# Kernel tuning notes

Measured on AMD Instinct MI355X. Metric: run time of the kernel, lower is better.

The kernel has to match this reference:

```python
import jax, jax.numpy as jnp
import numpy as np
import math

B, S, D, H, DH, DFF = 2, 2048, 2048, 16, 128, 8192
EPS = 1e-6
K_AMB = -1.0


def log_map_origin(x, K):
    # x: (..., d+1) Lorentz point -> tangent vector (..., d)
    xi = x[..., 1:]
    n = jnp.sqrt(jnp.sum(xi * xi, axis=-1, keepdims=True))
    a = jnp.sqrt(-K) * n
    # asinh(a)/a, stable near 0 (on-manifold, acosh(sqrt(-K)x0) == asinh(sqrt(-K)||xi||))
    f = jnp.where(a < 1e-6, 1.0 - a * a / 6.0, jnp.arcsinh(a) / jnp.maximum(a, 1e-12))
    return f * xi


def exp_map_stable(v, K):
    # v: (..., d) tangent -> Lorentz point (..., d+1); x0 from exact constraint
    n = jnp.sqrt(jnp.sum(v * v, axis=-1, keepdims=True))
    a = jnp.sqrt(-K) * n
    sinc = jnp.where(a < 1e-6, 1.0 + a * a / 6.0, jnp.sinh(a) / jnp.maximum(a, 1e-12))
    xi = sinc * v
    x0 = jnp.sqrt(-1.0 / K + jnp.sum(xi * xi, axis=-1, keepdims=True))
    return jnp.concatenate([x0, xi], axis=-1)


def lorentz_rmsnorm(x, scale):
    v = log_map_origin(x, K_AMB)
    rms = jnp.sqrt(jnp.mean(v * v, axis=-1, keepdims=True) + EPS)
    return exp_map_stable(scale * (v / rms), K_AMB)


def per_head_attention(x_normed, mask, Wq, Wk, Wv, Wo, head_K):
    v = log_map_origin(x_normed, K_AMB)  # (B,S,D)
    def split(w):
        return (v @ w).reshape(B, S, H, DH).transpose(0, 2, 1, 3)  # (B,H,S,DH)
    q, k, vv = split(Wq), split(Wk), split(Wv)
    Kh = head_K[None, :, None, None]  # (1,H,1,1) per-head curvature
    ql = exp_map_stable(q, Kh)  # (B,H,S,DH+1)
    kl = exp_map_stable(k, Kh)
    # Lorentz inner product <q,k>_L = -q0 k0 + qi.ki via signed metric
    metric = jnp.concatenate([-jnp.ones((1,)), jnp.ones((DH,))])
    L = jnp.einsum('bhqd,bhkd->bhqk', ql * metric, kl)
    # negative squared-distance proxy: 2<q,k>_L - 2/K  (zero when q==k)
    scores = (2.0 * L - 2.0 / Kh) / math.sqrt(DH)
    scores = jnp.where(mask[None, None, :, :], scores, -1e30)
    attn = jax.nn.softmax(scores, axis=-1)
    out = jnp.einsum('bhqk,bhkd->bhqd', attn, vv)  # (B,H,S,DH)
    out = out.transpose(0, 2, 1, 3).reshape(B, S, H * DH)
    return out @ Wo  # Euclidean (B,S,D)


def block_forward(x, mask, scale1, scale2, Wq, Wk, Wv, Wo, head_K, W1, W2):
    xn = lorentz_rmsnorm(x, scale1)
    attn_out = per_head_attention(xn, mask, Wq, Wk, Wv, Wo, head_K)
    x = exp_map_stable(log_map_origin(x, K_AMB) + attn_out, K_AMB)
    xn = lorentz_rmsnorm(x, scale2)
    vf = log_map_origin(xn, K_AMB)
    ffn_eu_pre = jax.nn.gelu(vf @ W1, approximate=False) @ W2
    ffn_out = exp_map_stable(ffn_eu_pre, K_AMB)
    x = exp_map_stable(log_map_origin(x, K_AMB) + log_map_origin(ffn_out, K_AMB), K_AMB)
    return x


def setup_inputs() -> dict:
    key = jax.random.key(0)
    ks = jax.random.split(key, 9)
    v0 = jax.random.normal(ks[0], (B, S, D), jnp.float32) * 0.02
    x = exp_map_stable(v0, K_AMB)  # on-manifold input (B,S,D+1)
    mask = jnp.tril(jnp.ones((S, S), bool))  # causal: True = attend
    init_scale = 1.0 / math.sqrt(D)
    w_std = 0.02
    return {
        'x': x,
        'mask': mask,
        'scale1': jnp.full((D,), init_scale, jnp.float32),
        'scale2': jnp.full((D,), init_scale, jnp.float32),
        'Wq': jax.random.normal(ks[1], (D, H * DH), jnp.float32) * w_std,
        'Wk': jax.random.normal(ks[2], (D, H * DH), jnp.float32) * w_std,
        'Wv': jax.random.normal(ks[3], (D, H * DH), jnp.float32) * w_std,
        'Wo': jax.random.normal(ks[4], (H * DH, D), jnp.float32) * w_std,
        'head_K': jnp.full((H,), -1.0, jnp.float32),
        'W1': jax.random.normal(ks[5], (D, DFF), jnp.float32) * w_std,
        'W2': jax.random.normal(ks[6], (DFF, D), jnp.float32) * w_std,
    }


def reference(x, mask, scale1, scale2, Wq, Wk, Wv, Wo, head_K, W1, W2):
    return block_forward(x, mask, scale1, scale2, Wq, Wk, Wv, Wo, head_K, W1, W2)
```

## Files before the change

### kernel.cpp

```cpp
#include <hip/hip_runtime.h>
#include <stdint.h>

typedef unsigned short u16;
typedef __attribute__((ext_vector_type(8))) short bf16x8;
typedef __attribute__((ext_vector_type(4))) float f32x4;

#define SEQ    2048
#define NB     2
#define NHEAD  16
#define DHEAD  128
#define DMODEL 2048
#define DFFN   8192
#define MROWS  4096

__device__ __forceinline__ u16 f2bf(float x) {
  union { float f; uint32_t u; } v; v.f = x;
  return (u16)((v.u + 0x7fffu + ((v.u >> 16) & 1u)) >> 16);
}
__device__ __forceinline__ float bf2f(u16 h) {
  union { uint32_t u; float f; } v; v.u = ((uint32_t)h) << 16;
  return v.f;
}
__device__ __forceinline__ void gload16(const void* g, void* l) {
  __builtin_amdgcn_global_load_lds((const __attribute__((address_space(1))) void*)g,
                                   (__attribute__((address_space(3))) void*)l,
                                   16, 0, 0);
}
__device__ __forceinline__ float blockSum256(float v) {
  __shared__ float red[4];
  #pragma unroll
  for (int m = 1; m < 64; m <<= 1) v += __shfl_xor(v, m, 64);
  int w = threadIdx.x >> 6;
  if ((threadIdx.x & 63) == 0) red[w] = v;
  __syncthreads();
  float s = red[0] + red[1] + red[2] + red[3];
  __syncthreads();
  return s;
}

__global__ void transpose_w(const float* __restrict__ in, u16* __restrict__ out, int R, int C) {
  __shared__ float tile[32][33];
  int c0 = blockIdx.x * 32, r0 = blockIdx.y * 32;
  int tx = threadIdx.x, ty = threadIdx.y;
  #pragma unroll
  for (int i = 0; i < 4; ++i)
    tile[ty + 8*i][tx] = in[(size_t)(r0 + ty + 8*i) * C + c0 + tx];
  __syncthreads();
  #pragma unroll
  for (int i = 0; i < 4; ++i)
    out[(size_t)(c0 + ty + 8*i) * R + r0 + tx] = f2bf(tile[tx][ty + 8*i]);
}

__global__ void ln_first(const float* __restrict__ x, const float* __restrict__ scale,
                         float* __restrict__ v1, u16* __restrict__ t1) {
  int row = blockIdx.x;
  const float* xr = x + (size_t)row * (DMODEL + 1) + 1;
  float vals[8]; float ss = 0.f;
  #pragma unroll
  for (int i = 0; i < 8; ++i) {
    int idx = threadIdx.x + 256 * i;
    vals[i] = xr[idx];
    ss += vals[i] * vals[i];
  }
  ss = blockSum256(ss);
  float n = sqrtf(ss);
  float f = (n < 1e-6f) ? (1.0f - n * n * (1.0f/6.0f)) : (asinhf(n) / n);
  float rms = sqrtf(f * f * ss * (1.0f / DMODEL) + 1e-6f);
  float ir = 1.0f / rms;
  #pragma unroll
  for (int i = 0; i < 8; ++i) {
    int idx = threadIdx.x + 256 * i;
    float v = f * vals[i];
    v1[(size_t)row * DMODEL + idx] = v;
    t1[(size_t)row * DMODEL + idx] = f2bf(scale[idx] * v * ir);
  }
}

__global__ void rms_mid(const float* __restrict__ u, const float* __restrict__ scale,
                        u16* __restrict__ t) {
  int row = blockIdx.x;
  const float* ur = u + (size_t)row * DMODEL;
  float vals[8]; float ss = 0.f;
  #pragma unroll
  for (int i = 0; i < 8; ++i) { int idx = threadIdx.x + 256*i; vals[i] = ur[idx]; ss += vals[i]*vals[i]; }
  ss = blockSum256(ss);
  float ir = 1.0f / sqrtf(ss * (1.0f / DMODEL) + 1e-6f);
  #pragma unroll
  for (int i = 0; i < 8; ++i) {
    int idx = threadIdx.x + 256*i;
    t[(size_t)row*DMODEL + idx] = f2bf(scale[idx]*vals[i]*ir);
  }
}

__global__ void final_exp(const float* __restrict__ u, float* __restrict__ out) {
  int row = blockIdx.x;
  const float* ur = u + (size_t)row * DMODEL;
  float vals[8]; float ss = 0.f;
  #pragma unroll
  for (int i = 0; i < 8; ++i) { int idx = threadIdx.x + 256*i; vals[i] = ur[idx]; ss += vals[i]*vals[i]; }
  ss = blockSum256(ss);
  float n = sqrtf(ss);
  float f = (n < 1e-6f) ? (1.0f + n*n*(1.0f/6.0f)) : (sinhf(n)/n);
  float* orow = out + (size_t)row * (DMODEL + 1);
  if (threadIdx.x == 0) orow[0] = sqrtf(1.0f + f*f*ss);
  #pragma unroll
  for (int i = 0; i < 8; ++i) { int idx = threadIdx.x + 256*i; orow[1+idx] = f*vals[i]; }
}

template<int EPI>
__global__ __launch_bounds__(512, 2) void gemm256(
    const u16* __restrict__ A, const u16* __restrict__ Bt,
    u16* __restrict__ Cb, float* Cf, const float* add,
    int M, int N, int K)
{
  __shared__ __attribute__((aligned(128))) char smem[131072];
  const int tid = threadIdx.x;
  const int w = tid >> 6, lane = tid & 63;
  const int lrow = lane & 15, kq = lane >> 4;
  const int wm = w >> 2, wn = w & 3;

  const int nwg = gridDim.x;
  const int cpx = nwg >> 3;
  const int sid = (blockIdx.x & 7) * cpx + (blockIdx.x >> 3);
  const int NX = N >> 8;
  const int bx = sid % NX, by = sid / NX;
  const int m0 = by * 256, n0 = bx * 256;
  const int NT = K >> 6;

  size_t goff[2];
  #pragma unroll
  for (int r = 0; r < 2; ++r) {
    int L = r * 8192 + tid * 16;
    int U = L ^ (((L >> 9) & 1) << 5);
    int si = U >> 10;
    int row = (si >> 1) * 16 + ((U >> 6) & 15);
    int col = (si & 1) * 32 + ((U & 63) >> 1);
    goff[r] = (size_t)row * K + col;
  }
  auto stage_half = [&](const u16* g, int ldsOff) {
    #pragma unroll
    for (int r = 0; r < 2; ++r)
      gload16(g + goff[r], smem + ldsOff + r * 8192 + w * 1024);
  };

  const u16* A0 = A  + (size_t)m0 * K;
  const u16* A1 = A  + (size_t)(m0 + 128) * K;
  const u16* B0 = Bt + (size_t)n0 * K;
  const u16* B1 = Bt + (size_t)(n0 + 128) * K;

  const int aoff = (lrow * 64 + kq * 16) ^ ((lrow & 8) << 2);

  f32x4 acc[8][4] = {};

  stage_half(A0, 0);
  stage_half(A1, 16384);
  stage_half(B0, 32768);
  stage_half(B1, 49152);
  stage_half(A0 + 64, 65536);
  stage_half(A1 + 64, 65536 + 16384);
  asm volatile("s_waitcnt vmcnt(4)" ::: "memory");
  asm volatile("s_barrier" ::: "memory");

  for (int t = 0; t < NT; ++t) {
    const int buf = t & 1;
    const char* ab = smem + buf * 65536 + wm * 16384 + aoff;
    const char* bb = smem + buf * 65536 + 32768 + (wn >> 1) * 16384 + (wn & 1) * 8192 + aoff;
    bf16x8 a0[4][2], a1[4][2], b0[2][2], b1[2][2];

    #pragma unroll
    for (int i = 0; i < 4; ++i)
      #pragma unroll
      for (int kk = 0; kk < 2; ++kk)
        a0[i][kk] = *(const bf16x8*)(ab + (i*2 + kk) * 1024);
    #pragma unroll
    for (int j = 0; j < 2; ++j)
      #pragma unroll
      for (int kk = 0; kk < 2; ++kk)
        b0[j][kk] = *(const bf16x8*)(bb + (j*2 + kk) * 1024);
    if (t + 1 < NT) stage_half(B0 + (t+1)*64, (buf^1)*65536 + 32768);
    asm volatile("s_barrier" ::: "memory");
    __builtin_amdgcn_s_setprio(1);
    #pragma unroll
    for (int kk = 0; kk < 2; ++kk)
      #pragma unroll
      for (int i = 0; i < 4; ++i)
        #pragma unroll
        for (int j = 0; j < 2; ++j)
          acc[i][j] = __builtin_amdgcn_mfma_f32_16x16x32_bf16(a0[i][kk], b0[j][kk], acc[i][j], 0, 0, 0);
    __builtin_amdgcn_s_setprio(0);
    asm volatile("s_barrier" ::: "memory");

    #pragma unroll
    for (int i = 0; i < 4; ++i)
      #pragma unroll
      for (int kk = 0; kk < 2; ++kk)
        a1[i][kk] = *(const bf16x8*)(ab + ((4 + i)*2 + kk) * 1024);
    if (t + 1 < NT) stage_half(B1 + (t+1)*64, (buf^1)*65536 + 49152);
    asm volatile("s_barrier" ::: "memory");
    __builtin_amdgcn_s_setprio(1);
    #pragma unroll
    for (int kk = 0; kk < 2; ++kk)
      #pragma unroll
      for (int i = 0; i < 4; ++i)
        #pragma unroll
        for (int j = 0; j < 2; ++j)
          acc[4 + i][j] = __builtin_amdgcn_mfma_f32_16x16x32_bf16(a1[i][kk], b0[j][kk], acc[4 + i][j], 0, 0, 0);
    __builtin_amdgcn_s_setprio(0);
    asm volatile("s_barrier" ::: "memory");

    #pragma unroll
    for (int j = 0; j < 2; ++j)
      #pragma unroll
      for (int kk = 0; kk < 2; ++kk)
        b1[j][kk] = *(const bf16x8*)(bb + ((2 + j)*2 + kk) * 1024);
    if (t + 2 < NT) stage_half(A0 + (t+2)*64, buf*65536);
    asm volatile("s_barrier" ::: "memory");
    __builtin_amdgcn_s_setprio(1);
    #pragma unroll
    for (int kk = 0; kk < 2; ++kk)
      #pragma unroll
      for (int i = 0; i < 4; ++i)
        #pragma unroll
        for (int j = 0; j < 2; ++j)
          acc[4 + i][2 + j] = __builtin_amdgcn_mfma_f32_16x16x32_bf16(a1[i][kk], b1[j][kk], acc[4 + i][2 + j], 0, 0, 0);
    __builtin_amdgcn_s_setprio(0);
    asm volatile("s_barrier" ::: "memory");

    if (t + 2 < NT) stage_half(A1 + (t+2)*64, buf*65536 + 16384);
    asm volatile("s_barrier" ::: "memory");
    __builtin_amdgcn_s_setprio(1);
    #pragma unroll
    for (int kk = 0; kk < 2; ++kk)
      #pragma unroll
      for (int i = 0; i < 4; ++i)
        #pragma unroll
        for (int j = 0; j < 2; ++j)
          acc[i][2 + j] = __builtin_amdgcn_mfma_f32_16x16x32_bf16(a0[i][kk], b1[j][kk], acc[i][2 + j], 0, 0, 0);
    __builtin_amdgcn_s_setprio(0);
    if (t + 2 < NT) asm volatile("s_waitcnt vmcnt(4)" ::: "memory");
    else            asm volatile("s_waitcnt vmcnt(0)" ::: "memory");
    asm volatile("s_barrier" ::: "memory");
  }

  #pragma unroll
  for (int i = 0; i < 8; ++i)
    #pragma unroll
    for (int j = 0; j < 4; ++j)
      #pragma unroll
      for (int r = 0; r < 4; ++r) {
        int row = m0 + wm*128 + i*16 + kq*4 + r;
        int col = n0 + wn*64 + j*16 + lrow;
        size_t idx = (size_t)row * N + col;
        float v = acc[i][j][r];
        if (EPI == 0) {
          Cb[idx] = f2bf(v);
        } else if (EPI == 1) {
          Cf[idx] = v + add[idx];
        } else {
          float g = 0.5f * v * (1.0f + erff(v * 0.70710678118654752f));
          Cb[idx] = f2bf(g);
        }
      }
}

__global__ void prep_qk(const u16* __restrict__ in, const float* __restrict__ headK,
                        u16* __restrict__ Lout, float* __restrict__ l0,
                        int instride, int off) {
  int gid = blockIdx.x * 4 + (threadIdx.x >> 6);
  int lane = threadIdx.x & 63;
  int b = gid >> 15;
  int rem = gid & 32767;
  int h = rem >> 11;
  int s = rem & 2047;
  const u16* src = in + ((size_t)(b * SEQ + s)) * instride + off + h * DHEAD + lane * 2;
  float v0 = bf2f(src[0]), v1 = bf2f(src[1]);
  float nn = v0*v0 + v1*v1;
  #pragma unroll
  for (int m = 1; m < 64; m <<= 1) nn += __shfl_xor(nn, m, 64);
  float Kh = headK[h];
  float sk = sqrtf(-Kh);
  float a = sk * sqrtf(nn);
  float f = (a < 1e-6f) ? (1.0f + a*a*(1.0f/6.0f)) : (sinhf(a) / a);
  u16* dst = Lout + (size_t)gid * DHEAD + lane * 2;
  dst[0] = f2bf(f * v0);
  dst[1] = f2bf(f * v1);
  if (lane == 0) l0[gid] = sqrtf(-1.0f/Kh + f*f*nn);
}

__global__ void vtrans(const u16* __restrict__ vb, u16* __restrict__ VT,
                       int instride, int off) {
  __shared__ u16 tile[32][33];
  int bh = blockIdx.x;
  int b = bh >> 4, h = bh & 15;
  int s0 = blockIdx.y * 32, d0 = blockIdx.z * 32;
  int tx = threadIdx.x, ty = threadIdx.y;
  #pragma unroll
  for (int i = 0; i < 4; ++i)
    tile[ty + 8*i][tx] = vb[((size_t)(b*SEQ + s0 + ty + 8*i)) * instride + off + h*DHEAD + d0 + tx];
  __syncthreads();
  #pragma unroll
  for (int i = 0; i < 4; ++i)
    VT[((size_t)bh*DHEAD + d0 + ty + 8*i) * SEQ + s0 + tx] = tile[tx][ty + 8*i];
}

__global__ __launch_bounds__(256, 2) void attn_kernel(
    const u16* __restrict__ Ql, const u16* __restrict__ Kl,
    const u16* __restrict__ VT, const float* __restrict__ ql0,
    const float* __restrict__ kl0, const float* __restrict__ headK,
    u16* __restrict__ out) {
  __shared__ u16 klds[2][32 * 128];
  __shared__ u16 vlds[2][128 * 32];
  __shared__ u16 plds[4][32 * 36];
  const int tid = threadIdx.x, w = tid >> 6, lane = tid & 63;
  const int lrow = lane & 15, kq = lane >> 4;
  const int id = blockIdx.x;
  const int bh = id & 31;
  const int qb = 15 - (id >> 5);
  const int q0 = qb * 128 + w * 32;
  const int b = bh >> 4, h = bh & 15;
  const float Kh = headK[h];
  const float LOG2E = 1.44269504088896f;
  const float isd = 0.088388347648318447f;
  const float sc_mul = 2.0f * isd * LOG2E;
  const float sc_add = (-2.0f / Kh) * isd * LOG2E;

  const u16* kbase  = Kl + (size_t)bh * SEQ * DHEAD;
  const u16* vtbase = VT + (size_t)bh * DHEAD * SEQ;
  const float* kl0b = kl0 + (size_t)bh * SEQ;
  u16* pw = &plds[w][0];

  bf16x8 aq[2][4];
  const u16* qbase = Ql + ((size_t)bh * SEQ + q0) * DHEAD;
  #pragma unroll
  for (int m = 0; m < 2; ++m)
    #pragma unroll
    for (int dc = 0; dc < 4; ++dc)
      aq[m][dc] = *(const bf16x8*)&qbase[(size_t)(m*16 + lrow) * DHEAD + dc*32 + kq*8];
  float q0r[2][4];
  #pragma unroll
  for (int m = 0; m < 2; ++m)
    #pragma unroll
    for (int r = 0; r < 4; ++r)
      q0r[m][r] = ql0[(size_t)bh * SEQ + q0 + m*16 + kq*4 + r];

  auto stage = [&](int k0, int buf) {
    #pragma unroll
    for (int i = 0; i < 2; ++i) {
      int rl = w*8 + i*4 + (lane >> 4);
      int c = (lane & 15) ^ (rl & 15);
      gload16(kbase + ((size_t)(k0 + rl)) * DHEAD + c * 8,
              &klds[buf][(w*8 + i*4) * 128]);
    }
    #pragma unroll
    for (int i = 0; i < 2; ++i) {
      int rl = w*32 + i*16 + (lane >> 2);
      int c = (lane & 3) ^ ((rl >> 1) & 3);
      gload16(vtbase + (size_t)rl * SEQ + k0 + c * 8,
              &vlds[buf][(w*32 + i*16) * 32]);
    }
  };

  float lacc[2][4] = {};
  f32x4 o[2][8] = {};
  const int niter = qb * 4 + 4;

  stage(0, 0);
  for (int i = 0; i < niter; ++i) {
    const int k0 = i * 32, buf = i & 1;
    float kc0 = kl0b[k0 + lrow];
    float kc1 = kl0b[k0 + 16 + lrow];
    if (i + 1 < niter) {
      stage(k0 + 32, buf ^ 1);
      asm volatile("s_waitcnt vmcnt(4)" ::: "memory");
    } else {
      asm volatile("s_waitcnt vmcnt(0)" ::: "memory");
    }
    asm volatile("s_barrier" ::: "memory");

    f32x4 sc[2][2] = {};
    #pragma unroll
    for (int dc = 0; dc < 4; ++dc) {
      int c = dc*4 + kq;
      bf16x8 bk0 = *(const bf16x8*)&klds[buf][lrow*128        + (c ^ (lrow & 15)) * 8];
      bf16x8 bk1 = *(const bf16x8*)&klds[buf][(16 + lrow)*128 + (c ^ ((16 + lrow) & 15)) * 8];
      #pragma unroll
      for (int m = 0; m < 2; ++m) {
        sc[m][0] = __builtin_amdgcn_mfma_f32_16x16x32_bf16(aq[m][dc], bk0, sc[m][0], 0, 0, 0);
        sc[m][1] = __builtin_amdgcn_mfma_f32_16x16x32_bf16(aq[m][dc], bk1, sc[m][1], 0, 0, 0);
      }
    }
    #pragma unroll
    for (int m = 0; m < 2; ++m)
      #pragma unroll
      for (int r = 0; r < 4; ++r) {
        int qg = q0 + m*16 + kq*4 + r;
        float p0 = exp2f((sc[m][0][r] - q0r[m][r] * kc0) * sc_mul + sc_add);
        float p1 = exp2f((sc[m][1][r] - q0r[m][r] * kc1) * sc_mul + sc_add);
        p0 = (k0 + lrow      <= qg) ? p0 : 0.f;
        p1 = (k0 + 16 + lrow <= qg) ? p1 : 0.f;
        lacc[m][r] += p0 + p1;
        pw[(m*16 + kq*4 + r) * 36 + lrow]      = f2bf(p0);
        pw[(m*16 + kq*4 + r) * 36 + 16 + lrow] = f2bf(p1);
      }
    bf16x8 ap0 = *(const bf16x8*)&pw[(size_t)lrow * 36 + kq*8];
    bf16x8 ap1 = *(const bf16x8*)&pw[(size_t)(16 + lrow) * 36 + kq*8];
    int vc = (kq ^ ((lrow >> 1) & 3)) * 8;
    #pragma unroll
    for (int n = 0; n < 8; ++n) {
      bf16x8 bv = *(const bf16x8*)&vlds[buf][(n*16 + lrow) * 32 + vc];
      o[0][n] = __builtin_amdgcn_mfma_f32_16x16x32_bf16(ap0, bv, o[0][n], 0, 0, 0);
      o[1][n] = __builtin_amdgcn_mfma_f32_16x16x32_bf16(ap1, bv, o[1][n], 0, 0, 0);
    }
    asm volatile("s_barrier" ::: "memory");
  }

  float rcl[2][4];
  #pragma unroll
  for (int m = 0; m < 2; ++m)
    #pragma unroll
    for (int r = 0; r < 4; ++r) {
      float s = lacc[m][r];
      #pragma unroll
      for (int mm = 1; mm < 16; mm <<= 1) s += __shfl_xor(s, mm, 16);
      rcl[m][r] = 1.0f / s;
    }
  #pragma unroll
  for (int m = 0; m < 2; ++m)
    #pragma unroll
    for (int n = 0; n < 8; ++n)
      #pragma unroll
      for (int r = 0; r < 4; ++r) {
        int qg = q0 + m*16 + kq*4 + r;
        out[((size_t)b * SEQ + qg) * DMODEL + h * DHEAD + n*16 + lrow] =
            f2bf(o[m][n][r] * rcl[m][r]);
      }
}

extern "C" void kernel_launch(void* const* d_in, const int* in_sizes, int n_in,
                              void* d_out, int out_size, void* d_ws, size_t ws_size,
                              hipStream_t stream) {
  const float* x      = (const float*)d_in[0];
  const float* scale1 = (const float*)d_in[2];
  const float* scale2 = (const float*)d_in[3];
  const float* Wq     = (const float*)d_in[4];
  const float* Wk     = (const float*)d_in[5];
  const float* Wv     = (const float*)d_in[6];
  const float* Wo     = (const float*)d_in[7];
  const float* headK  = (const float*)d_in[8];
  const float* W1     = (const float*)d_in[9];
  const float* W2     = (const float*)d_in[10];
  float* out = (float*)d_out;

  char* p = (char*)d_ws;
  size_t off = 0;
  auto take = [&](size_t bytes) -> char* {
    char* r = p + off;
    off += (bytes + 255) & ~(size_t)255;
    return r;
  };
  u16* WqT = (u16*)take((size_t)DMODEL*DMODEL*2);
  u16* WkT = (u16*)take((size_t)DMODEL*DMODEL*2);
  u16* WvT = (u16*)take((size_t)DMODEL*DMODEL*2);
  u16* WoT = (u16*)take((size_t)DMODEL*DMODEL*2);
  u16* W1T = (u16*)take((size_t)DMODEL*DFFN*2);
  u16* W2T = (u16*)take((size_t)DMODEL*DFFN*2);
  float* vres = (float*)take((size_t)MROWS*DMODEL*4);
  u16* tbuf = (u16*)take((size_t)MROWS*DMODEL*2);
  u16* qkvb = (u16*)take((size_t)MROWS*3*DMODEL*2);
  u16* Qlb  = (u16*)take((size_t)MROWS*DMODEL*2);
  u16* Klb  = (u16*)take((size_t)MROWS*DMODEL*2);
  u16* VTb  = (u16*)take((size_t)MROWS*DMODEL*2);
  float* q0b = (float*)take((size_t)NB*NHEAD*SEQ*4);
  float* k0b = (float*)take((size_t)NB*NHEAD*SEQ*4);
  u16* hbuf = qkvb;
  u16* attnout = tbuf;

  dim3 tb(32, 8);
  transpose_w<<<dim3(DMODEL/32, DMODEL/32), tb, 0, stream>>>(Wq, WqT, DMODEL, DMODEL);
  transpose_w<<<dim3(DMODEL/32, DMODEL/32), tb, 0, stream>>>(Wk, WkT, DMODEL, DMODEL);
  transpose_w<<<dim3(DMODEL/32, DMODEL/32), tb, 0, stream>>>(Wv, WvT, DMODEL, DMODEL);
  transpose_w<<<dim3(DMODEL/32, DMODEL/32), tb, 0, stream>>>(Wo, WoT, DMODEL, DMODEL);
  transpose_w<<<dim3(DFFN/32,   DMODEL/32), tb, 0, stream>>>(W1, W1T, DMODEL, DFFN);
  transpose_w<<<dim3(DMODEL/32, DFFN/32),   tb, 0, stream>>>(W2, W2T, DFFN, DMODEL);

  ln_first<<<MROWS, 256, 0, stream>>>(x, scale1, vres, tbuf);

  gemm256<0><<<dim3((3*DMODEL/256)*(MROWS/256)), 512, 0, stream>>>(
      tbuf, WqT, qkvb, nullptr, nullptr, MROWS, 3*DMODEL, DMODEL);

  prep_qk<<<NB*NHEAD*SEQ/4, 256, 0, stream>>>(qkvb, headK, Qlb, q0b, 3*DMODEL, 0);
  prep_qk<<<NB*NHEAD*SEQ/4, 256, 0, stream>>>(qkvb, headK, Klb, k0b, 3*DMODEL, DMODEL);
  vtrans<<<dim3(NB*NHEAD, SEQ/32, DHEAD/32), tb, 0, stream>>>(qkvb, VTb, 3*DMODEL, 2*DMODEL);

  attn_kernel<<<dim3(512), 256, 0, stream>>>(Qlb, Klb, VTb, q0b, k0b, headK, attnout);

  gemm256<1><<<dim3((DMODEL/256)*(MROWS/256)), 512, 0, stream>>>(
      attnout, WoT, nullptr, vres, vres, MROWS, DMODEL, DMODEL);

  rms_mid<<<MROWS, 256, 0, stream>>>(vres, scale2, tbuf);

  gemm256<2><<<dim3((DFFN/256)*(MROWS/256)), 512, 0, stream>>>(
      tbuf, W1T, hbuf, nullptr, nullptr, MROWS, DFFN, DMODEL);

  gemm256<1><<<dim3((DMODEL/256)*(MROWS/256)), 512, 0, stream>>>(
      hbuf, W2T, nullptr, vres, vres, MROWS, DMODEL, DFFN);

  final_exp<<<MROWS, 256, 0, stream>>>(vres, out);

  (void)in_sizes; (void)n_in; (void)out_size; (void)ws_size;
}
```

Measured before the change: 1.003 ms.

## Split-K the Wo and W2 GEMMs, summing partials in the norm kernels

The two N=2048 GEMMs (output projection and FFN down-projection) now run as split-K=2 over a second grid dimension. Each half writes fp32 partials into reused scratch buffers, and the partials plus the residual are summed inside rms_mid3 and final_exp3. The goal is to double the workgroup count for these GEMMs, which otherwise launch only 128 tiles. In exchange they write and read extra full-size fp32 partial buffers, and the scratch aliasing relies on buffers such as the transposed weights being dead by then.

```diff
diff --git a/kernel.cpp b/kernel.cpp
--- a/kernel.cpp
+++ b/kernel.cpp
@@ -76,28 +76,39 @@
   }
 }
 
-__global__ void rms_mid(const float* __restrict__ u, const float* __restrict__ scale,
-                        u16* __restrict__ t) {
+__global__ void rms_mid3(float* __restrict__ u, const float* __restrict__ p0,
+                         const float* __restrict__ p1, const float* __restrict__ scale,
+                         u16* __restrict__ t) {
   int row = blockIdx.x;
-  const float* ur = u + (size_t)row * DMODEL;
+  size_t base = (size_t)row * DMODEL;
   float vals[8]; float ss = 0.f;
   #pragma unroll
-  for (int i = 0; i < 8; ++i) { int idx = threadIdx.x + 256*i; vals[i] = ur[idx]; ss += vals[i]*vals[i]; }
+  for (int i = 0; i < 8; ++i) {
+    int idx = threadIdx.x + 256*i;
+    float v = u[base + idx] + p0[base + idx] + p1[base + idx];
+    vals[i] = v; ss += v*v;
+  }
   ss = blockSum256(ss);
   float ir = 1.0f / sqrtf(ss * (1.0f / DMODEL) + 1e-6f);
   #pragma unroll
   for (int i = 0; i < 8; ++i) {
     int idx = threadIdx.x + 256*i;
-    t[(size_t)row*DMODEL + idx] = f2bf(scale[idx]*vals[i]*ir);
-  }
-}
-
-__global__ void final_exp(const float* __restrict__ u, float* __restrict__ out) {
+    u[base + idx] = vals[i];
+    t[base + idx] = f2bf(scale[idx]*vals[i]*ir);
+  }
+}
+
+__global__ void final_exp3(const float* __restrict__ u, const float* __restrict__ p0,
+                           const float* __restrict__ p1, float* __restrict__ out) {
   int row = blockIdx.x;
-  const float* ur = u + (size_t)row * DMODEL;
+  size_t base = (size_t)row * DMODEL;
   float vals[8]; float ss = 0.f;
   #pragma unroll
-  for (int i = 0; i < 8; ++i) { int idx = threadIdx.x + 256*i; vals[i] = ur[idx]; ss += vals[i]*vals[i]; }
+  for (int i = 0; i < 8; ++i) {
+    int idx = threadIdx.x + 256*i;
+    float v = u[base + idx] + p0[base + idx] + p1[base + idx];
+    vals[i] = v; ss += v*v;
+  }
   ss = blockSum256(ss);
   float n = sqrtf(ss);
   float f = (n < 1e-6f) ? (1.0f + n*n*(1.0f/6.0f)) : (sinhf(n)/n);
@@ -110,8 +121,8 @@
 template<int EPI>
 __global__ __launch_bounds__(512, 2) void gemm256(
     const u16* __restrict__ A, const u16* __restrict__ Bt,
-    u16* __restrict__ Cb, float* Cf, const float* add,
-    int M, int N, int K)
+    u16* __restrict__ Cb, float* Cf,
+    int M, int N, int K, int kHalf)
 {
   __shared__ __attribute__((aligned(128))) char smem[131072];
   const int tid = threadIdx.x;
@@ -119,13 +130,18 @@
   const int lrow = lane & 15, kq = lane >> 4;
   const int wm = w >> 2, wn = w & 3;
 
+  const int ksel = blockIdx.y;
+  A  += (size_t)ksel * kHalf;
+  Bt += (size_t)ksel * kHalf;
+  if (EPI == 3) Cf += (size_t)ksel * M * N;
+  const int NT = kHalf >> 6;
+
   const int nwg = gridDim.x;
   const int cpx = nwg >> 3;
   const int sid = (blockIdx.x & 7) * cpx + (blockIdx.x >> 3);
   const int NX = N >> 8;
   const int bx = sid % NX, by = sid / NX;
   const int m0 = by * 256, n0 = bx * 256;
-  const int NT = K >> 6;
 
   size_t goff[2];
   #pragma unroll
@@ -254,8 +270,8 @@
         float v = acc[i][j][r];
         if (EPI == 0) {
           Cb[idx] = f2bf(v);
-        } else if (EPI == 1) {
-          Cf[idx] = v + add[idx];
+        } else if (EPI == 3) {
+          Cf[idx] = v;
         } else {
           float g = 0.5f * v * (1.0f + erff(v * 0.70710678118654752f));
           Cb[idx] = f2bf(g);
@@ -475,6 +491,11 @@
   u16* hbuf = qkvb;
   u16* attnout = tbuf;
 
+  float* PoA = (float*)qkvb;
+  float* PoB = PoA + (size_t)MROWS*DMODEL;
+  float* PfA = (float*)WqT;
+  float* PfB = (float*)Klb;
+
   dim3 tb(32, 8);
   transpose_w<<<dim3(DMODEL/32, DMODEL/32), tb, 0, stream>>>(Wq, WqT, DMODEL, DMODEL);
   transpose_w<<<dim3(DMODEL/32, DMODEL/32), tb, 0, stream>>>(Wk, WkT, DMODEL, DMODEL);
@@ -485,8 +506,8 @@
 
   ln_first<<<MROWS, 256, 0, stream>>>(x, scale1, vres, tbuf);
 
-  gemm256<0><<<dim3((3*DMODEL/256)*(MROWS/256)), 512, 0, stream>>>(
-      tbuf, WqT, qkvb, nullptr, nullptr, MROWS, 3*DMODEL, DMODEL);
+  gemm256<0><<<dim3((3*DMODEL/256)*(MROWS/256), 1), 512, 0, stream>>>(
+      tbuf, WqT, qkvb, nullptr, MROWS, 3*DMODEL, DMODEL, DMODEL);
 
   prep_qk<<<NB*NHEAD*SEQ/4, 256, 0, stream>>>(qkvb, headK, Qlb, q0b, 3*DMODEL, 0);
   prep_qk<<<NB*NHEAD*SEQ/4, 256, 0, stream>>>(qkvb, headK, Klb, k0b, 3*DMODEL, DMODEL);
@@ -494,18 +515,18 @@
 
   attn_kernel<<<dim3(512), 256, 0, stream>>>(Qlb, Klb, VTb, q0b, k0b, headK, attnout);
 
-  gemm256<1><<<dim3((DMODEL/256)*(MROWS/256)), 512, 0, stream>>>(
-      attnout, WoT, nullptr, vres, vres, MROWS, DMODEL, DMODEL);
-
-  rms_mid<<<MROWS, 256, 0, stream>>>(vres, scale2, tbuf);
-
-  gemm256<2><<<dim3((DFFN/256)*(MROWS/256)), 512, 0, stream>>>(
-      tbuf, W1T, hbuf, nullptr, nullptr, MROWS, DFFN, DMODEL);
-
-  gemm256<1><<<dim3((DMODEL/256)*(MROWS/256)), 512, 0, stream>>>(
-      hbuf, W2T, nullptr, vres, vres, MROWS, DMODEL, DFFN);
-
-  final_exp<<<MROWS, 256, 0, stream>>>(vres, out);
-
-  (void)in_sizes; (void)n_in; (void)out_size; (void)ws_size;
-}
+  gemm256<3><<<dim3((DMODEL/256)*(MROWS/256), 2), 512, 0, stream>>>(
+      attnout, WoT, nullptr, PoA, MROWS, DMODEL, DMODEL, DMODEL/2);
+
+  rms_mid3<<<MROWS, 256, 0, stream>>>(vres, PoA, PoB, scale2, tbuf);
+
+  gemm256<2><<<dim3((DFFN/256)*(MROWS/256), 1), 512, 0, stream>>>(
+      tbuf, W1T, hbuf, nullptr, MROWS, DFFN, DMODEL, DMODEL);
+
+  gemm256<3><<<dim3((DMODEL/256)*(MROWS/256), 2), 512, 0, stream>>>(
+      hbuf, W2T, nullptr, PfA, MROWS, DMODEL, DFFN, DFFN/2);
+
+  final_exp3<<<MROWS, 256, 0, stream>>>(vres, PfA, (float*)W1T, out);
+
+  (void)PfB; (void)in_sizes; (void)n_in; (void)out_size; (void)ws_size;
+}
```

After: 905.1 us. -9.7%, faster.
